# Optimization experiments

Hardware: AMD Instinct MI355X
Metric: run time of the kernel (lower is better)

## Reference

```python
import jax, jax.numpy as jnp
import numpy as np

N_EMBD = 1024
N_HEAD = 16
B, T = 1, 4096
EPS = 1e-5


def layer_norm(x, w):
    mu = jnp.mean(x, axis=-1, keepdims=True)
    var = jnp.var(x, axis=-1, keepdims=True)
    return (x - mu) / jnp.sqrt(var + EPS) * w


def setup_inputs() -> dict:
    key = jax.random.key(0)
    ks = jax.random.split(key, 6)
    s = 0.02
    return {
        "x": jax.random.normal(ks[0], (B, T, N_EMBD), dtype=jnp.float32),
        "w_qkv": jax.random.normal(ks[1], (N_EMBD, 3 * N_EMBD), dtype=jnp.float32) * s,
        "w_attn_proj": jax.random.normal(ks[2], (N_EMBD, N_EMBD), dtype=jnp.float32) * s,
        "w_fc": jax.random.normal(ks[3], (N_EMBD, 4 * N_EMBD), dtype=jnp.float32) * s,
        "w_mlp_proj": jax.random.normal(ks[4], (4 * N_EMBD, N_EMBD), dtype=jnp.float32) * s,
        "ln1_w": jnp.ones((N_EMBD,), dtype=jnp.float32),
        "ln2_w": jnp.ones((N_EMBD,), dtype=jnp.float32),
    }


def reference(x, w_qkv, w_attn_proj, w_fc, w_mlp_proj, ln1_w, ln2_w):
    Bq, Tq, C = x.shape
    hs = C // N_HEAD

    # --- attention branch (pre-norm) ---
    h = layer_norm(x, ln1_w)
    qkv = h @ w_qkv  # [B,T,3C]
    q, k, v = jnp.split(qkv, 3, axis=-1)
    q = q.reshape(Bq, Tq, N_HEAD, hs).transpose(0, 2, 1, 3)  # [B,H,T,hs]
    k = k.reshape(Bq, Tq, N_HEAD, hs).transpose(0, 2, 1, 3)
    v = v.reshape(Bq, Tq, N_HEAD, hs).transpose(0, 2, 1, 3)

    scores = jnp.einsum("bhqd,bhkd->bhqk", q, k) * (1.0 / jnp.sqrt(jnp.float32(hs)))
    causal = jnp.tril(jnp.ones((Tq, Tq), dtype=bool))
    scores = jnp.where(causal, scores, -jnp.inf)
    weights = jax.nn.softmax(scores, axis=-1)  # dropout=0 -> identity
    out = jnp.einsum("bhqk,bhkd->bhqd", weights, v)
    out = out.transpose(0, 2, 1, 3).reshape(Bq, Tq, C)
    x = x + out @ w_attn_proj

    # --- MLP branch (pre-norm) ---
    h = layer_norm(x, ln2_w)
    h = jax.nn.gelu(h @ w_fc, approximate=False)  # nn.GELU default is exact
    x = x + h @ w_mlp_proj
    return x
```

## Files before the change

kernel.cpp:

```cpp
#include <hip/hip_runtime.h>
#include <cstdint>

typedef __attribute__((ext_vector_type(8))) short short8;
typedef __attribute__((ext_vector_type(4))) float f32x4;
typedef __attribute__((ext_vector_type(4))) unsigned int u32x4;

__device__ __forceinline__ float b2f(unsigned short u) {
    return __uint_as_float(((unsigned int)u) << 16);
}
__device__ __forceinline__ unsigned short f2b(float f) {
    unsigned int u = __float_as_uint(f);
    u += 0x7FFFu + ((u >> 16) & 1u);
    return (unsigned short)(u >> 16);
}

__global__ __launch_bounds__(256) void k_transpose_all(
        const float* __restrict__ w0, const float* __restrict__ w1,
        const float* __restrict__ w2, const float* __restrict__ w3,
        unsigned short* __restrict__ o0, unsigned short* __restrict__ o1,
        unsigned short* __restrict__ o2, unsigned short* __restrict__ o3) {
    __shared__ float tile[32][33];
    int b = blockIdx.x;
    const float* w; unsigned short* o; int K, N, nx, tb;
    if (b < 3072)      { w = w0; o = o0; K = 1024; N = 3072; nx = 96;  tb = b; }
    else if (b < 4096) { w = w1; o = o1; K = 1024; N = 1024; nx = 32;  tb = b - 3072; }
    else if (b < 8192) { w = w2; o = o2; K = 1024; N = 4096; nx = 128; tb = b - 4096; }
    else               { w = w3; o = o3; K = 4096; N = 1024; nx = 32;  tb = b - 8192; }
    int n0 = (tb % nx) * 32, k0 = (tb / nx) * 32;
    int tx = threadIdx.x, ty = threadIdx.y;
#pragma unroll
    for (int i = 0; i < 4; i++)
        tile[ty + 8 * i][tx] = w[(size_t)(k0 + ty + 8 * i) * N + n0 + tx];
    __syncthreads();
#pragma unroll
    for (int i = 0; i < 4; i++)
        o[(size_t)(n0 + ty + 8 * i) * K + k0 + tx] = f2b(tile[tx][ty + 8 * i]);
}

__global__ __launch_bounds__(256) void k_layernorm(
        const float* __restrict__ x, const float* __restrict__ w,
        unsigned short* __restrict__ out) {
    int row = blockIdx.x, tid = threadIdx.x;
    const float4* xr = (const float4*)(x + (size_t)row * 1024);
    float4 v = xr[tid];
    float s  = v.x + v.y + v.z + v.w;
    float ss = v.x * v.x + v.y * v.y + v.z * v.z + v.w * v.w;
#pragma unroll
    for (int off = 32; off >= 1; off >>= 1) {
        s  += __shfl_down(s, off);
        ss += __shfl_down(ss, off);
    }
    __shared__ float red[10];
    if ((tid & 63) == 0) { red[tid >> 6] = s; red[4 + (tid >> 6)] = ss; }
    __syncthreads();
    if (tid == 0) {
        float S  = red[0] + red[1] + red[2] + red[3];
        float SS = red[4] + red[5] + red[6] + red[7];
        float mu  = S * (1.0f / 1024.0f);
        float var = SS * (1.0f / 1024.0f) - mu * mu;
        red[8] = mu; red[9] = rsqrtf(var + 1e-5f);
    }
    __syncthreads();
    float mu = red[8], rs = red[9];
    float4 wv = ((const float4*)w)[tid];
    ushort4 pk;
    pk.x = f2b((v.x - mu) * rs * wv.x);
    pk.y = f2b((v.y - mu) * rs * wv.y);
    pk.z = f2b((v.z - mu) * rs * wv.z);
    pk.w = f2b((v.w - mu) * rs * wv.w);
    *(ushort4*)(out + (size_t)row * 1024 + tid * 4) = pk;
}

__global__ __launch_bounds__(256) void k_reduce(
        const float* __restrict__ res, const float* __restrict__ p0,
        const float* __restrict__ p1, float* __restrict__ out, int n4) {
    int i = blockIdx.x * 256 + threadIdx.x;
    if (i < n4) {
        float4 a = ((const float4*)res)[i];
        float4 b = ((const float4*)p0)[i];
        float4 c = ((const float4*)p1)[i];
        a.x += b.x + c.x; a.y += b.y + c.y; a.z += b.z + c.z; a.w += b.w + c.w;
        ((float4*)out)[i] = a;
    }
}

template <int EPI, int TM, int TN, int MINW>
__global__ __launch_bounds__(256, MINW) void k_gemm_bt(
        const unsigned short* __restrict__ A, const unsigned short* __restrict__ BT,
        const float* __restrict__ RES, void* __restrict__ OUT,
        int M, int N, int K) {
    constexpr int WT = (TM == 128) ? 64 : 32;
    constexpr int MI = WT / 16;
    constexpr int NA = TM / 32, NB = TN / 32;
    __shared__ __align__(16) unsigned short As[TM * 64];
    __shared__ __align__(16) unsigned short Bs[TN * 64];
    int tid  = threadIdx.x;
    int lane = tid & 63, wave = tid >> 6;
    int quad = lane >> 4, qr = lane & 15;
    int wm_off = (wave >> 1) * WT;
    int wn_off = (wave & 1) * WT;
    int m0 = blockIdx.y * TM, n0 = blockIdx.x * TN;
    int ks = K / gridDim.z;
    int kbeg = blockIdx.z * ks;
    int r0 = tid >> 3;
    int c0 = (tid & 7) * 8;
    int cs = 8 * (((tid & 7) + (r0 & 7)) & 7);
    int cswz[2];
#pragma unroll
    for (int kk = 0; kk < 2; kk++) cswz[kk] = 8 * (((kk * 4) + quad + (qr & 7)) & 7);

    const unsigned short* Ap = A  + (size_t)(m0 + r0) * K + kbeg + c0;
    const unsigned short* Bp = BT + (size_t)(n0 + r0) * K + kbeg + c0;
    const size_t sA = (size_t)32 * K;

    uint4 pa0, pa1, pa2, pa3, pb0, pb1, pb2, pb3;
    pa0 = *(const uint4*)(Ap);
    pa1 = *(const uint4*)(Ap + sA);
    if constexpr (NA == 4) {
        pa2 = *(const uint4*)(Ap + 2 * sA);
        pa3 = *(const uint4*)(Ap + 3 * sA);
    }
    pb0 = *(const uint4*)(Bp);
    pb1 = *(const uint4*)(Bp + sA);
    if constexpr (NB == 4) {
        pb2 = *(const uint4*)(Bp + 2 * sA);
        pb3 = *(const uint4*)(Bp + 3 * sA);
    }

    f32x4 acc[MI][MI] = {};
    for (int k0 = 0; k0 < ks; k0 += 64) {
        __syncthreads();
        *(uint4*)&As[(r0)      * 64 + cs] = pa0;
        *(uint4*)&As[(32 + r0) * 64 + cs] = pa1;
        if constexpr (NA == 4) {
            *(uint4*)&As[(64 + r0) * 64 + cs] = pa2;
            *(uint4*)&As[(96 + r0) * 64 + cs] = pa3;
        }
        *(uint4*)&Bs[(r0)      * 64 + cs] = pb0;
        *(uint4*)&Bs[(32 + r0) * 64 + cs] = pb1;
        if constexpr (NB == 4) {
            *(uint4*)&Bs[(64 + r0) * 64 + cs] = pb2;
            *(uint4*)&Bs[(96 + r0) * 64 + cs] = pb3;
        }
        __syncthreads();
        if (k0 + 64 < ks) {
            int k = k0 + 64;
            pa0 = *(const uint4*)(Ap + k);
            pa1 = *(const uint4*)(Ap + sA + k);
            if constexpr (NA == 4) {
                pa2 = *(const uint4*)(Ap + 2 * sA + k);
                pa3 = *(const uint4*)(Ap + 3 * sA + k);
            }
            pb0 = *(const uint4*)(Bp + k);
            pb1 = *(const uint4*)(Bp + sA + k);
            if constexpr (NB == 4) {
                pb2 = *(const uint4*)(Bp + 2 * sA + k);
                pb3 = *(const uint4*)(Bp + 3 * sA + k);
            }
        }
#pragma unroll
        for (int kk = 0; kk < 2; kk++) {
            short8 af[MI], bfr[MI];
#pragma unroll
            for (int i = 0; i < MI; i++) af[i]  = *(const short8*)&As[(wm_off + i * 16 + qr) * 64 + cswz[kk]];
#pragma unroll
            for (int j = 0; j < MI; j++) bfr[j] = *(const short8*)&Bs[(wn_off + j * 16 + qr) * 64 + cswz[kk]];
#pragma unroll
            for (int i = 0; i < MI; i++)
#pragma unroll
                for (int j = 0; j < MI; j++)
                    acc[i][j] = __builtin_amdgcn_mfma_f32_16x16x32_bf16(af[i], bfr[j], acc[i][j], 0, 0, 0);
        }
    }
    float* outz = (EPI == 0) ? ((float*)OUT + (size_t)blockIdx.z * M * N) : (float*)OUT;
#pragma unroll
    for (int i = 0; i < MI; i++) {
#pragma unroll
        for (int j = 0; j < MI; j++) {
#pragma unroll
            for (int r = 0; r < 4; r++) {
                int row = m0 + wm_off + i * 16 + quad * 4 + r;
                int col = n0 + wn_off + j * 16 + qr;
                size_t idx = (size_t)row * N + col;
                float v = acc[i][j][r];
                if (EPI == 0)      outz[idx] = v;
                else if (EPI == 1) ((unsigned short*)OUT)[idx] = f2b(v);
                else if (EPI == 2) ((float*)OUT)[idx] = RES[idx] + v;
                else {
                    float u = v * fmaf(v * v, 0.035677408f, 0.79788456f);
                    float e = fminf(u * 2.885390082f, 80.0f);
                    float t = exp2f(e);
                    float g = v * t / (t + 1.0f);
                    ((unsigned short*)OUT)[idx] = f2b(g);
                }
            }
        }
    }
}

__global__ __launch_bounds__(256, 4) void k_attn(
        const unsigned short* __restrict__ qkv, unsigned short* __restrict__ out) {
    __shared__ unsigned short Ks[128][72];
    __shared__ unsigned short Vt[64][136];

    const float C1 = 0.18033688f;
    const float C2 = 5.77078016f;

    int l = blockIdx.x;
    int h = l & 15;
    int qb = 63 - (l >> 4);
    int q0 = qb * 64;

    int tid = threadIdx.x;
    int wave = tid >> 6, lane = tid & 63;
    int lane16 = lane & 15, quad = lane >> 4;
    int qrow = q0 + wave * 16 + lane16;

    {
        int srow = tid >> 2, sc0 = (tid & 3) * 16;
        size_t base = (size_t)(q0 + srow) * 3072 + h * 64 + sc0;
        *(uint4*)&Ks[srow][sc0]     = *(const uint4*)&qkv[base];
        *(uint4*)&Ks[srow][sc0 + 8] = *(const uint4*)&qkv[base + 8];
    }
    __syncthreads();
    short8 aq0 = *(const short8*)&Ks[wave * 16 + lane16][quad * 8];
    short8 aq1 = *(const short8*)&Ks[wave * 16 + lane16][32 + quad * 8];

    f32x4 Oacc[4] = {};
    float lsum = 0.f;

    int srow = tid >> 1, sc0 = (tid & 1) * 32;
    int vk = (lane & 31) * 2;
    int d0 = wave * 16 + (lane >> 5) * 8;
    int u  = lane & 15;
    int tt = ((u & 6) << 1) | ((u & 8) >> 2) | (u & 1);
    int dstc = (lane & 16) * 2 + 2 * tt;

    uint4 pk0, pk1, pk2, pk3, pv0, pv1, pv2, pv3;
    {
        size_t base = (size_t)srow * 3072 + 1024 + h * 64 + sc0;
        pk0 = *(const uint4*)&qkv[base];
        pk1 = *(const uint4*)&qkv[base + 8];
        pk2 = *(const uint4*)&qkv[base + 16];
        pk3 = *(const uint4*)&qkv[base + 24];
        size_t vb0 = (size_t)vk * 3072 + 2048 + h * 64 + d0;
        pv0 = *(const uint4*)&qkv[vb0];
        pv1 = *(const uint4*)&qkv[vb0 + 3072];
        size_t vb1 = (size_t)(64 + vk) * 3072 + 2048 + h * 64 + d0;
        pv2 = *(const uint4*)&qkv[vb1];
        pv3 = *(const uint4*)&qkv[vb1 + 3072];
    }

    for (int kc = 0; kc <= qb; kc += 2) {
        __syncthreads();
        {
            *(uint4*)&Ks[srow][sc0]      = pk0;
            *(uint4*)&Ks[srow][sc0 + 8]  = pk1;
            *(uint4*)&Ks[srow][sc0 + 16] = pk2;
            *(uint4*)&Ks[srow][sc0 + 24] = pk3;
        }
        {
            const unsigned short* pe0 = (const unsigned short*)&pv0;
            const unsigned short* po0 = (const unsigned short*)&pv1;
            const unsigned short* pe1 = (const unsigned short*)&pv2;
            const unsigned short* po1 = (const unsigned short*)&pv3;
#pragma unroll
            for (int j = 0; j < 8; j++) {
                *(uint32_t*)&Vt[d0 + j][dstc]      = (uint32_t)pe0[j] | ((uint32_t)po0[j] << 16);
                *(uint32_t*)&Vt[d0 + j][64 + dstc] = (uint32_t)pe1[j] | ((uint32_t)po1[j] << 16);
            }
        }
        __syncthreads();

        if (kc + 2 <= qb) {
            size_t base = (size_t)((kc + 2) * 64 + srow) * 3072 + 1024 + h * 64 + sc0;
            pk0 = *(const uint4*)&qkv[base];
            pk1 = *(const uint4*)&qkv[base + 8];
            pk2 = *(const uint4*)&qkv[base + 16];
            pk3 = *(const uint4*)&qkv[base + 24];
            size_t vb0 = (size_t)((kc + 2) * 64 + vk) * 3072 + 2048 + h * 64 + d0;
            pv0 = *(const uint4*)&qkv[vb0];
            pv1 = *(const uint4*)&qkv[vb0 + 3072];
            size_t vb1 = (size_t)((kc + 3) * 64 + vk) * 3072 + 2048 + h * 64 + d0;
            pv2 = *(const uint4*)&qkv[vb1];
            pv3 = *(const uint4*)&qkv[vb1 + 3072];
        }

        f32x4 sacc[8] = {};
#pragma unroll
        for (int kt = 0; kt < 8; kt++) {
            short8 bk0 = *(const short8*)&Ks[kt * 16 + lane16][quad * 8];
            short8 bk1 = *(const short8*)&Ks[kt * 16 + lane16][32 + quad * 8];
            sacc[kt] = __builtin_amdgcn_mfma_f32_16x16x32_bf16(bk0, aq0, sacc[kt], 0, 0, 0);
            sacc[kt] = __builtin_amdgcn_mfma_f32_16x16x32_bf16(bk1, aq1, sacc[kt], 0, 0, 0);
        }

        bool domask = (kc + 2 > qb);
        short8 ap[4];
#pragma unroll
        for (int s = 0; s < 4; s++) {
            u32x4 w;
#pragma unroll
            for (int hh = 0; hh < 2; hh++) {
                int kt = 2 * s + hh;
                float pr[4];
#pragma unroll
                for (int r = 0; r < 4; r++) {
                    float sc = sacc[kt][r];
                    if (domask) {
                        int key = kc * 64 + kt * 16 + quad * 4 + r;
                        sc = (key <= qrow) ? sc : -__builtin_inff();
                    }
                    float p = exp2f(fmaf(sc, C1, -C2));
                    lsum += p;
                    pr[r] = p;
                }
                uint32_t w0 = (__float_as_uint(pr[0]) >> 16) | (__float_as_uint(pr[1]) & 0xFFFF0000u);
                uint32_t w1 = (__float_as_uint(pr[2]) >> 16) | (__float_as_uint(pr[3]) & 0xFFFF0000u);
                if (hh == 0) { w.x = w0; w.y = w1; } else { w.z = w0; w.w = w1; }
            }
            ap[s] = __builtin_bit_cast(short8, w);
        }

#pragma unroll
        for (int s = 0; s < 4; s++) {
#pragma unroll
            for (int dt = 0; dt < 4; dt++) {
                short8 bv = *(const short8*)&Vt[dt * 16 + lane16][s * 32 + quad * 8];
                Oacc[dt] = __builtin_amdgcn_mfma_f32_16x16x32_bf16(ap[s], bv, Oacc[dt], 0, 0, 0);
            }
        }
    }

    float lf = lsum;
    lf += __shfl_xor(lf, 16);
    lf += __shfl_xor(lf, 32);
    float invl[4];
#pragma unroll
    for (int r = 0; r < 4; r++) invl[r] = 1.0f / __shfl(lf, quad * 4 + r);
#pragma unroll
    for (int dt = 0; dt < 4; dt++) {
#pragma unroll
        for (int r = 0; r < 4; r++) {
            int qr_out = q0 + wave * 16 + quad * 4 + r;
            out[(size_t)qr_out * 1024 + h * 64 + dt * 16 + lane16] = f2b(Oacc[dt][r] * invl[r]);
        }
    }
}

extern "C" void kernel_launch(void* const* d_in, const int* in_sizes, int n_in,
                              void* d_out, int out_size, void* d_ws, size_t ws_size,
                              hipStream_t stream) {
    const float* x      = (const float*)d_in[0];
    const float* w_qkv  = (const float*)d_in[1];
    const float* w_attn = (const float*)d_in[2];
    const float* w_fc   = (const float*)d_in[3];
    const float* w_mlp  = (const float*)d_in[4];
    const float* ln1w   = (const float*)d_in[5];
    const float* ln2w   = (const float*)d_in[6];

    char* ws = (char*)d_ws;
    unsigned short* h      = (unsigned short*)(ws + 0);
    unsigned short* wqkvT  = (unsigned short*)(ws + 8388608);
    unsigned short* wattnT = (unsigned short*)(ws + 14680064);
    unsigned short* wfcT   = (unsigned short*)(ws + 16777216);
    unsigned short* wmlpT  = (unsigned short*)(ws + 25165824);
    unsigned short* qkv    = (unsigned short*)(ws + 33554432);
    unsigned short* attno  = (unsigned short*)(ws + 58720256);
    float*          x2     = (float*)(ws + 67108864);
    unsigned short* fcact  = (unsigned short*)(ws + 83886080);
    float* pA = (float*)(ws + 83886080);
    float* pM = (float*)(ws + 33554432);
    float* outF = (float*)d_out;

    k_transpose_all<<<12288, dim3(32, 8), 0, stream>>>(
        w_qkv, w_attn, w_fc, w_mlp, wqkvT, wattnT, wfcT, wmlpT);

    k_layernorm<<<4096, 256, 0, stream>>>(x, ln1w, h);
    k_gemm_bt<1, 128, 128, 3><<<dim3(24, 32), 256, 0, stream>>>(h, wqkvT, nullptr, qkv, 4096, 3072, 1024);
    k_attn<<<1024, 256, 0, stream>>>(qkv, attno);
    k_gemm_bt<0, 128, 128, 3><<<dim3(8, 32, 2), 256, 0, stream>>>(attno, wattnT, nullptr, pA, 4096, 1024, 1024);
    k_reduce<<<4096, 256, 0, stream>>>(x, pA, pA + 4194304, x2, 1048576);
    k_layernorm<<<4096, 256, 0, stream>>>(x2, ln2w, h);
    k_gemm_bt<3, 128, 128, 3><<<dim3(32, 32), 256, 0, stream>>>(h, wfcT, nullptr, fcact, 4096, 4096, 1024);
    k_gemm_bt<0, 128, 128, 3><<<dim3(8, 32, 2), 256, 0, stream>>>(fcact, wmlpT, nullptr, pM, 4096, 1024, 4096);
    k_reduce<<<4096, 256, 0, stream>>>(x2, pM, pM + 4194304, outF, 1048576);
}
```

Baseline: 373.6 us.

## Swizzle attention K/V shared-memory layout, rebalance causal block order, add MFMA priority

Replaces the padded K and transposed-V shared-memory arrays with unpadded XOR-swizzled layouts and rewrites the global-load and transpose-store indexing to match, using v_perm to pack V pairs. The aim is to avoid LDS bank conflicts and padding waste. It also reorders the causal query-block schedule into interleaved short and long blocks to balance work across CUs, and raises wave priority around the MFMA loops. The swizzle indexing is intricate and could cause correctness or conflict regressions.

```diff
diff --git a/kernel.cpp b/kernel.cpp
--- a/kernel.cpp
+++ b/kernel.cpp
@@ -200,15 +200,18 @@
 
 __global__ __launch_bounds__(256, 4) void k_attn(
         const unsigned short* __restrict__ qkv, unsigned short* __restrict__ out) {
-    __shared__ unsigned short Ks[128][72];
-    __shared__ unsigned short Vt[64][136];
+    __shared__ __align__(16) unsigned short Ks[128 * 64];
+    __shared__ __align__(16) unsigned short Vt[64 * 128];
 
     const float C1 = 0.18033688f;
     const float C2 = 5.77078016f;
 
     int l = blockIdx.x;
     int h = l & 15;
-    int qb = 63 - (l >> 4);
+    int idx = l >> 4;
+    int kk_ = idx & 15, hi_ = idx >> 4;
+    int qb = (hi_ == 0) ? (2 * kk_) : (hi_ == 1) ? (63 - 2 * kk_)
+           : (hi_ == 2) ? (31 - 2 * kk_) : (32 + 2 * kk_);
     int q0 = qb * 64;
 
     int tid = threadIdx.x;
@@ -217,83 +220,95 @@
     int qrow = q0 + wave * 16 + lane16;
 
     {
-        int srow = tid >> 2, sc0 = (tid & 3) * 16;
-        size_t base = (size_t)(q0 + srow) * 3072 + h * 64 + sc0;
-        *(uint4*)&Ks[srow][sc0]     = *(const uint4*)&qkv[base];
-        *(uint4*)&Ks[srow][sc0 + 8] = *(const uint4*)&qkv[base + 8];
+        int srow = tid >> 2;
+        int c1 = 2 * (tid & 3);
+        int p1 = c1 ^ (srow & 7), p2 = (c1 | 1) ^ (srow & 7);
+        size_t base = (size_t)(q0 + srow) * 3072 + h * 64 + c1 * 8;
+        *(uint4*)&Ks[srow * 64 + p1 * 8] = *(const uint4*)&qkv[base];
+        *(uint4*)&Ks[srow * 64 + p2 * 8] = *(const uint4*)&qkv[base + 8];
     }
     __syncthreads();
-    short8 aq0 = *(const short8*)&Ks[wave * 16 + lane16][quad * 8];
-    short8 aq1 = *(const short8*)&Ks[wave * 16 + lane16][32 + quad * 8];
+    short8 aq0, aq1;
+    {
+        int pq = quad ^ (lane16 & 7);
+        const unsigned short* qr_ = &Ks[(wave * 16 + lane16) * 64];
+        aq0 = *(const short8*)&qr_[pq * 8];
+        aq1 = *(const short8*)&qr_[(pq ^ 4) * 8];
+    }
 
     f32x4 Oacc[4] = {};
     float lsum = 0.f;
 
-    int srow = tid >> 1, sc0 = (tid & 1) * 32;
-    int vk = (lane & 31) * 2;
-    int d0 = wave * 16 + (lane >> 5) * 8;
-    int u  = lane & 15;
-    int tt = ((u & 6) << 1) | ((u & 8) >> 2) | (u & 1);
-    int dstc = (lane & 16) * 2 + 2 * tt;
-
-    uint4 pk0, pk1, pk2, pk3, pv0, pv1, pv2, pv3;
+    int a_ = lane >> 3, b_ = lane & 7;
+    size_t kgbase = (size_t)(wave * 32 + a_) * 3072 + 1024 + h * 64 + ((b_ ^ a_) << 3);
+    int    kwbase = (wave * 32 + a_) * 64 + b_ * 8;
+    size_t vgbase = (size_t)(wave * 32 + 2 * a_) * 3072 + 2048 + h * 64 + (b_ << 3);
+    int tt0 = ((a_ & 6) << 1) | (a_ & 1);
+    int pc0 = wave * 16 + tt0, pc1 = pc0 + 2;
+    int vo0 = ((((pc0 >> 2) ^ b_) & 15) << 4) | ((pc0 & 3) << 2);
+    int vo1 = ((((pc1 >> 2) ^ b_) & 15) << 4) | ((pc1 & 3) << 2);
+
+    uint4 pk0, pk1, pk2, pk3, pvE0, pvO0, pvE1, pvO1;
     {
-        size_t base = (size_t)srow * 3072 + 1024 + h * 64 + sc0;
-        pk0 = *(const uint4*)&qkv[base];
-        pk1 = *(const uint4*)&qkv[base + 8];
-        pk2 = *(const uint4*)&qkv[base + 16];
-        pk3 = *(const uint4*)&qkv[base + 24];
-        size_t vb0 = (size_t)vk * 3072 + 2048 + h * 64 + d0;
-        pv0 = *(const uint4*)&qkv[vb0];
-        pv1 = *(const uint4*)&qkv[vb0 + 3072];
-        size_t vb1 = (size_t)(64 + vk) * 3072 + 2048 + h * 64 + d0;
-        pv2 = *(const uint4*)&qkv[vb1];
-        pv3 = *(const uint4*)&qkv[vb1 + 3072];
+        pk0 = *(const uint4*)&qkv[kgbase];
+        pk1 = *(const uint4*)&qkv[kgbase + 24576];
+        pk2 = *(const uint4*)&qkv[kgbase + 49152];
+        pk3 = *(const uint4*)&qkv[kgbase + 73728];
+        pvE0 = *(const uint4*)&qkv[vgbase];
+        pvO0 = *(const uint4*)&qkv[vgbase + 3072];
+        pvE1 = *(const uint4*)&qkv[vgbase + 49152];
+        pvO1 = *(const uint4*)&qkv[vgbase + 49152 + 3072];
     }
 
     for (int kc = 0; kc <= qb; kc += 2) {
         __syncthreads();
         {
-            *(uint4*)&Ks[srow][sc0]      = pk0;
-            *(uint4*)&Ks[srow][sc0 + 8]  = pk1;
-            *(uint4*)&Ks[srow][sc0 + 16] = pk2;
-            *(uint4*)&Ks[srow][sc0 + 24] = pk3;
+            *(uint4*)&Ks[kwbase]        = pk0;
+            *(uint4*)&Ks[kwbase + 512]  = pk1;
+            *(uint4*)&Ks[kwbase + 1024] = pk2;
+            *(uint4*)&Ks[kwbase + 1536] = pk3;
         }
         {
-            const unsigned short* pe0 = (const unsigned short*)&pv0;
-            const unsigned short* po0 = (const unsigned short*)&pv1;
-            const unsigned short* pe1 = (const unsigned short*)&pv2;
-            const unsigned short* po1 = (const unsigned short*)&pv3;
-#pragma unroll
-            for (int j = 0; j < 8; j++) {
-                *(uint32_t*)&Vt[d0 + j][dstc]      = (uint32_t)pe0[j] | ((uint32_t)po0[j] << 16);
-                *(uint32_t*)&Vt[d0 + j][64 + dstc] = (uint32_t)pe1[j] | ((uint32_t)po1[j] << 16);
+            const uint32_t* e0 = (const uint32_t*)&pvE0;
+            const uint32_t* o0 = (const uint32_t*)&pvO0;
+            const uint32_t* e1 = (const uint32_t*)&pvE1;
+            const uint32_t* o1 = (const uint32_t*)&pvO1;
+            char* vt = (char*)Vt + b_ * 8 * 256;
+#pragma unroll
+            for (int j = 0; j < 4; j++) {
+                *(uint32_t*)(vt + (2 * j) * 256     + vo0) = __builtin_amdgcn_perm(o0[j], e0[j], 0x05040100u);
+                *(uint32_t*)(vt + (2 * j + 1) * 256 + vo0) = __builtin_amdgcn_perm(o0[j], e0[j], 0x07060302u);
+                *(uint32_t*)(vt + (2 * j) * 256     + vo1) = __builtin_amdgcn_perm(o1[j], e1[j], 0x05040100u);
+                *(uint32_t*)(vt + (2 * j + 1) * 256 + vo1) = __builtin_amdgcn_perm(o1[j], e1[j], 0x07060302u);
             }
         }
         __syncthreads();
 
         if (kc + 2 <= qb) {
-            size_t base = (size_t)((kc + 2) * 64 + srow) * 3072 + 1024 + h * 64 + sc0;
-            pk0 = *(const uint4*)&qkv[base];
-            pk1 = *(const uint4*)&qkv[base + 8];
-            pk2 = *(const uint4*)&qkv[base + 16];
-            pk3 = *(const uint4*)&qkv[base + 24];
-            size_t vb0 = (size_t)((kc + 2) * 64 + vk) * 3072 + 2048 + h * 64 + d0;
-            pv0 = *(const uint4*)&qkv[vb0];
-            pv1 = *(const uint4*)&qkv[vb0 + 3072];
-            size_t vb1 = (size_t)((kc + 3) * 64 + vk) * 3072 + 2048 + h * 64 + d0;
-            pv2 = *(const uint4*)&qkv[vb1];
-            pv3 = *(const uint4*)&qkv[vb1 + 3072];
+            size_t kb = kgbase + (size_t)(kc + 2) * 196608;
+            pk0 = *(const uint4*)&qkv[kb];
+            pk1 = *(const uint4*)&qkv[kb + 24576];
+            pk2 = *(const uint4*)&qkv[kb + 49152];
+            pk3 = *(const uint4*)&qkv[kb + 73728];
+            size_t vb = vgbase + (size_t)(kc + 2) * 196608;
+            pvE0 = *(const uint4*)&qkv[vb];
+            pvO0 = *(const uint4*)&qkv[vb + 3072];
+            pvE1 = *(const uint4*)&qkv[vb + 49152];
+            pvO1 = *(const uint4*)&qkv[vb + 49152 + 3072];
         }
 
         f32x4 sacc[8] = {};
+        __builtin_amdgcn_s_setprio(1);
 #pragma unroll
         for (int kt = 0; kt < 8; kt++) {
-            short8 bk0 = *(const short8*)&Ks[kt * 16 + lane16][quad * 8];
-            short8 bk1 = *(const short8*)&Ks[kt * 16 + lane16][32 + quad * 8];
+            int ph = quad ^ (lane16 & 7);
+            const unsigned short* krow = &Ks[(kt * 16 + lane16) * 64];
+            short8 bk0 = *(const short8*)&krow[ph * 8];
+            short8 bk1 = *(const short8*)&krow[(ph ^ 4) * 8];
             sacc[kt] = __builtin_amdgcn_mfma_f32_16x16x32_bf16(bk0, aq0, sacc[kt], 0, 0, 0);
             sacc[kt] = __builtin_amdgcn_mfma_f32_16x16x32_bf16(bk1, aq1, sacc[kt], 0, 0, 0);
         }
+        __builtin_amdgcn_s_setprio(0);
 
         bool domask = (kc + 2 > qb);
         short8 ap[4];
@@ -322,14 +337,18 @@
             ap[s] = __builtin_bit_cast(short8, w);
         }
 
+        __builtin_amdgcn_s_setprio(1);
 #pragma unroll
         for (int s = 0; s < 4; s++) {
 #pragma unroll
             for (int dt = 0; dt < 4; dt++) {
-                short8 bv = *(const short8*)&Vt[dt * 16 + lane16][s * 32 + quad * 8];
+                int dv = dt * 16 + lane16;
+                int blk = (4 * s + quad) ^ (dv >> 3);
+                short8 bv = *(const short8*)((const char*)Vt + dv * 256 + blk * 16);
                 Oacc[dt] = __builtin_amdgcn_mfma_f32_16x16x32_bf16(ap[s], bv, Oacc[dt], 0, 0, 0);
             }
         }
+        __builtin_amdgcn_s_setprio(0);
     }
 
     float lf = lsum;
```

Result: slower. 409.3 us (+9.6%).

## Split attention keys across waves with cross-wave reduction and balanced block order

Applied to the files above, without the earlier changes.

Attention now assigns each wave a 32-key slice of every 128-key chunk for all 64 query rows, instead of 16 query rows against all keys. K is fed to the MFMAs straight from global memory into registers. V is double-buffered in LDS with one barrier per chunk, and the partial outputs and row sums are reduced across waves through LDS at the end. Query blocks are reordered so that long and short causal blocks interleave, and s_setprio hints are added around the MFMA sections. The aim is fewer barriers, no K staging, and better load balance, at the cost of more registers (occupancy hint lowered from 4 to 2) and a serialized final reduction.

```diff
diff --git a/kernel.cpp b/kernel.cpp
--- a/kernel.cpp
+++ b/kernel.cpp
@@ -198,152 +198,215 @@
     }
 }
 
-__global__ __launch_bounds__(256, 4) void k_attn(
+__global__ __launch_bounds__(256, 2) void k_attn(
         const unsigned short* __restrict__ qkv, unsigned short* __restrict__ out) {
-    __shared__ unsigned short Ks[128][72];
-    __shared__ unsigned short Vt[64][136];
+    __shared__ __align__(16) unsigned short Vt[2][64][136];
+    __shared__ float lred[4][64];
 
     const float C1 = 0.18033688f;
     const float C2 = 5.77078016f;
 
     int l = blockIdx.x;
     int h = l & 15;
-    int qb = 63 - (l >> 4);
+    int idx = l >> 4;
+    int kk_ = idx & 15, hi_ = idx >> 4;
+    int qb = (hi_ == 0) ? (2 * kk_) : (hi_ == 1) ? (63 - 2 * kk_)
+           : (hi_ == 2) ? (31 - 2 * kk_) : (32 + 2 * kk_);
     int q0 = qb * 64;
+    int lastc = qb >> 1;
 
     int tid = threadIdx.x;
     int wave = tid >> 6, lane = tid & 63;
     int lane16 = lane & 15, quad = lane >> 4;
-    int qrow = q0 + wave * 16 + lane16;
-
-    {
-        int srow = tid >> 2, sc0 = (tid & 3) * 16;
-        size_t base = (size_t)(q0 + srow) * 3072 + h * 64 + sc0;
-        *(uint4*)&Ks[srow][sc0]     = *(const uint4*)&qkv[base];
-        *(uint4*)&Ks[srow][sc0 + 8] = *(const uint4*)&qkv[base + 8];
-    }
-    __syncthreads();
-    short8 aq0 = *(const short8*)&Ks[wave * 16 + lane16][quad * 8];
-    short8 aq1 = *(const short8*)&Ks[wave * 16 + lane16][32 + quad * 8];
-
-    f32x4 Oacc[4] = {};
-    float lsum = 0.f;
-
-    int srow = tid >> 1, sc0 = (tid & 1) * 32;
+
+    size_t kbase = (size_t)(wave * 32 + lane16) * 3072 + 1024 + h * 64 + quad * 8;
+    size_t qbase = (size_t)(q0 + lane16) * 3072 + h * 64 + quad * 8;
     int vk = (lane & 31) * 2;
     int d0 = wave * 16 + (lane >> 5) * 8;
-    int u  = lane & 15;
+    size_t vgbase = (size_t)vk * 3072 + 2048 + h * 64 + d0;
+    int u = lane & 15;
     int tt = ((u & 6) << 1) | ((u & 8) >> 2) | (u & 1);
     int dstc = (lane & 16) * 2 + 2 * tt;
 
-    uint4 pk0, pk1, pk2, pk3, pv0, pv1, pv2, pv3;
+    uint4 pvE0 = *(const uint4*)&qkv[vgbase];
+    uint4 pvO0 = *(const uint4*)&qkv[vgbase + 3072];
+    uint4 pvE1 = *(const uint4*)&qkv[vgbase + 196608];
+    uint4 pvO1 = *(const uint4*)&qkv[vgbase + 196608 + 3072];
+    uint4 kp00 = *(const uint4*)&qkv[kbase];
+    uint4 kp01 = *(const uint4*)&qkv[kbase + 32];
+    uint4 kp10 = *(const uint4*)&qkv[kbase + 49152];
+    uint4 kp11 = *(const uint4*)&qkv[kbase + 49152 + 32];
+    short8 aq[4][2];
+#pragma unroll
+    for (int g = 0; g < 4; g++) {
+        aq[g][0] = __builtin_bit_cast(short8, *(const uint4*)&qkv[qbase + g * 49152]);
+        aq[g][1] = __builtin_bit_cast(short8, *(const uint4*)&qkv[qbase + g * 49152 + 32]);
+    }
     {
-        size_t base = (size_t)srow * 3072 + 1024 + h * 64 + sc0;
-        pk0 = *(const uint4*)&qkv[base];
-        pk1 = *(const uint4*)&qkv[base + 8];
-        pk2 = *(const uint4*)&qkv[base + 16];
-        pk3 = *(const uint4*)&qkv[base + 24];
-        size_t vb0 = (size_t)vk * 3072 + 2048 + h * 64 + d0;
-        pv0 = *(const uint4*)&qkv[vb0];
-        pv1 = *(const uint4*)&qkv[vb0 + 3072];
-        size_t vb1 = (size_t)(64 + vk) * 3072 + 2048 + h * 64 + d0;
-        pv2 = *(const uint4*)&qkv[vb1];
-        pv3 = *(const uint4*)&qkv[vb1 + 3072];
-    }
-
-    for (int kc = 0; kc <= qb; kc += 2) {
+        const unsigned short* pe0 = (const unsigned short*)&pvE0;
+        const unsigned short* po0 = (const unsigned short*)&pvO0;
+        const unsigned short* pe1 = (const unsigned short*)&pvE1;
+        const unsigned short* po1 = (const unsigned short*)&pvO1;
+#pragma unroll
+        for (int j = 0; j < 8; j++) {
+            *(uint32_t*)&Vt[0][d0 + j][dstc]      = (uint32_t)pe0[j] | ((uint32_t)po0[j] << 16);
+            *(uint32_t*)&Vt[0][d0 + j][64 + dstc] = (uint32_t)pe1[j] | ((uint32_t)po1[j] << 16);
+        }
+    }
+    if (lastc >= 1) {
+        size_t vb = vgbase + 393216;
+        pvE0 = *(const uint4*)&qkv[vb];
+        pvO0 = *(const uint4*)&qkv[vb + 3072];
+        pvE1 = *(const uint4*)&qkv[vb + 196608];
+        pvO1 = *(const uint4*)&qkv[vb + 196608 + 3072];
+    }
+
+    f32x4 Oacc[4][4] = {};
+    float lsum[4] = {0.f, 0.f, 0.f, 0.f};
+
+    for (int c = 0; c <= lastc; ++c) {
+        int cur = c & 1;
         __syncthreads();
-        {
-            *(uint4*)&Ks[srow][sc0]      = pk0;
-            *(uint4*)&Ks[srow][sc0 + 8]  = pk1;
-            *(uint4*)&Ks[srow][sc0 + 16] = pk2;
-            *(uint4*)&Ks[srow][sc0 + 24] = pk3;
-        }
-        {
-            const unsigned short* pe0 = (const unsigned short*)&pv0;
-            const unsigned short* po0 = (const unsigned short*)&pv1;
-            const unsigned short* pe1 = (const unsigned short*)&pv2;
-            const unsigned short* po1 = (const unsigned short*)&pv3;
+
+        f32x4 sacc[2][4];
+        __builtin_amdgcn_s_setprio(1);
+#pragma unroll
+        for (int kg = 0; kg < 2; kg++) {
+            short8 a0 = __builtin_bit_cast(short8, kg ? kp10 : kp00);
+            short8 a1 = __builtin_bit_cast(short8, kg ? kp11 : kp01);
+#pragma unroll
+            for (int g = 0; g < 4; g++) {
+                f32x4 s = {};
+                s = __builtin_amdgcn_mfma_f32_16x16x32_bf16(a0, aq[g][0], s, 0, 0, 0);
+                s = __builtin_amdgcn_mfma_f32_16x16x32_bf16(a1, aq[g][1], s, 0, 0, 0);
+                sacc[kg][g] = s;
+            }
+        }
+        __builtin_amdgcn_s_setprio(0);
+
+        if (c < lastc) {
+            const unsigned short* pe0 = (const unsigned short*)&pvE0;
+            const unsigned short* po0 = (const unsigned short*)&pvO0;
+            const unsigned short* pe1 = (const unsigned short*)&pvE1;
+            const unsigned short* po1 = (const unsigned short*)&pvO1;
 #pragma unroll
             for (int j = 0; j < 8; j++) {
-                *(uint32_t*)&Vt[d0 + j][dstc]      = (uint32_t)pe0[j] | ((uint32_t)po0[j] << 16);
-                *(uint32_t*)&Vt[d0 + j][64 + dstc] = (uint32_t)pe1[j] | ((uint32_t)po1[j] << 16);
-            }
-        }
-        __syncthreads();
-
-        if (kc + 2 <= qb) {
-            size_t base = (size_t)((kc + 2) * 64 + srow) * 3072 + 1024 + h * 64 + sc0;
-            pk0 = *(const uint4*)&qkv[base];
-            pk1 = *(const uint4*)&qkv[base + 8];
-            pk2 = *(const uint4*)&qkv[base + 16];
-            pk3 = *(const uint4*)&qkv[base + 24];
-            size_t vb0 = (size_t)((kc + 2) * 64 + vk) * 3072 + 2048 + h * 64 + d0;
-            pv0 = *(const uint4*)&qkv[vb0];
-            pv1 = *(const uint4*)&qkv[vb0 + 3072];
-            size_t vb1 = (size_t)((kc + 3) * 64 + vk) * 3072 + 2048 + h * 64 + d0;
-            pv2 = *(const uint4*)&qkv[vb1];
-            pv3 = *(const uint4*)&qkv[vb1 + 3072];
-        }
-
-        f32x4 sacc[8] = {};
-#pragma unroll
-        for (int kt = 0; kt < 8; kt++) {
-            short8 bk0 = *(const short8*)&Ks[kt * 16 + lane16][quad * 8];
-            short8 bk1 = *(const short8*)&Ks[kt * 16 + lane16][32 + quad * 8];
-            sacc[kt] = __builtin_amdgcn_mfma_f32_16x16x32_bf16(bk0, aq0, sacc[kt], 0, 0, 0);
-            sacc[kt] = __builtin_amdgcn_mfma_f32_16x16x32_bf16(bk1, aq1, sacc[kt], 0, 0, 0);
-        }
-
-        bool domask = (kc + 2 > qb);
+                *(uint32_t*)&Vt[cur ^ 1][d0 + j][dstc]      = (uint32_t)pe0[j] | ((uint32_t)po0[j] << 16);
+                *(uint32_t*)&Vt[cur ^ 1][d0 + j][64 + dstc] = (uint32_t)pe1[j] | ((uint32_t)po1[j] << 16);
+            }
+        }
+        if (c < lastc) {
+            size_t kb = kbase + (size_t)(c + 1) * 393216;
+            kp00 = *(const uint4*)&qkv[kb];
+            kp01 = *(const uint4*)&qkv[kb + 32];
+            kp10 = *(const uint4*)&qkv[kb + 49152];
+            kp11 = *(const uint4*)&qkv[kb + 49152 + 32];
+        }
+        if (c + 2 <= lastc) {
+            size_t vb = vgbase + (size_t)(c + 2) * 393216;
+            pvE0 = *(const uint4*)&qkv[vb];
+            pvO0 = *(const uint4*)&qkv[vb + 3072];
+            pvE1 = *(const uint4*)&qkv[vb + 196608];
+            pvO1 = *(const uint4*)&qkv[vb + 196608 + 3072];
+        }
+
+        int keybase = c * 128 + wave * 32;
+        bool domask = (keybase + 31 > q0);
         short8 ap[4];
 #pragma unroll
-        for (int s = 0; s < 4; s++) {
+        for (int g = 0; g < 4; g++) {
+            int qrow = q0 + g * 16 + lane16;
             u32x4 w;
 #pragma unroll
-            for (int hh = 0; hh < 2; hh++) {
-                int kt = 2 * s + hh;
+            for (int kg = 0; kg < 2; kg++) {
                 float pr[4];
 #pragma unroll
                 for (int r = 0; r < 4; r++) {
-                    float sc = sacc[kt][r];
+                    float sc = sacc[kg][g][r];
                     if (domask) {
-                        int key = kc * 64 + kt * 16 + quad * 4 + r;
+                        int key = keybase + kg * 16 + quad * 4 + r;
                         sc = (key <= qrow) ? sc : -__builtin_inff();
                     }
                     float p = exp2f(fmaf(sc, C1, -C2));
-                    lsum += p;
+                    lsum[g] += p;
                     pr[r] = p;
                 }
                 uint32_t w0 = (__float_as_uint(pr[0]) >> 16) | (__float_as_uint(pr[1]) & 0xFFFF0000u);
                 uint32_t w1 = (__float_as_uint(pr[2]) >> 16) | (__float_as_uint(pr[3]) & 0xFFFF0000u);
-                if (hh == 0) { w.x = w0; w.y = w1; } else { w.z = w0; w.w = w1; }
-            }
-            ap[s] = __builtin_bit_cast(short8, w);
-        }
-
-#pragma unroll
-        for (int s = 0; s < 4; s++) {
-#pragma unroll
-            for (int dt = 0; dt < 4; dt++) {
-                short8 bv = *(const short8*)&Vt[dt * 16 + lane16][s * 32 + quad * 8];
-                Oacc[dt] = __builtin_amdgcn_mfma_f32_16x16x32_bf16(ap[s], bv, Oacc[dt], 0, 0, 0);
-            }
-        }
-    }
-
-    float lf = lsum;
-    lf += __shfl_xor(lf, 16);
-    lf += __shfl_xor(lf, 32);
-    float invl[4];
-#pragma unroll
-    for (int r = 0; r < 4; r++) invl[r] = 1.0f / __shfl(lf, quad * 4 + r);
-#pragma unroll
-    for (int dt = 0; dt < 4; dt++) {
-#pragma unroll
-        for (int r = 0; r < 4; r++) {
-            int qr_out = q0 + wave * 16 + quad * 4 + r;
-            out[(size_t)qr_out * 1024 + h * 64 + dt * 16 + lane16] = f2b(Oacc[dt][r] * invl[r]);
+                if (kg == 0) { w.x = w0; w.y = w1; } else { w.z = w0; w.w = w1; }
+            }
+            ap[g] = __builtin_bit_cast(short8, w);
+        }
+
+        __builtin_amdgcn_s_setprio(1);
+#pragma unroll
+        for (int dt = 0; dt < 4; dt++) {
+            short8 bv = *(const short8*)&Vt[cur][dt * 16 + lane16][wave * 32 + quad * 8];
+#pragma unroll
+            for (int g = 0; g < 4; g++)
+                Oacc[g][dt] = __builtin_amdgcn_mfma_f32_16x16x32_bf16(ap[g], bv, Oacc[g][dt], 0, 0, 0);
+        }
+        __builtin_amdgcn_s_setprio(0);
+    }
+
+#pragma unroll
+    for (int g = 0; g < 4; g++) {
+        float lf = lsum[g];
+        lf += __shfl_xor(lf, 16);
+        lf += __shfl_xor(lf, 32);
+        lsum[g] = lf;
+    }
+    if (quad == 0) {
+#pragma unroll
+        for (int g = 0; g < 4; g++) lred[wave][g * 16 + lane16] = lsum[g];
+    }
+    __syncthreads();
+
+    float* Obuf = (float*)&Vt[0][0][0];
+    if (wave == 3) {
+#pragma unroll
+        for (int g = 0; g < 4; g++)
+#pragma unroll
+            for (int dt = 0; dt < 4; dt++)
+#pragma unroll
+                for (int r = 0; r < 4; r++)
+                    Obuf[(g * 16 + quad * 4 + r) * 68 + dt * 16 + lane16] = Oacc[g][dt][r];
+    }
+    __syncthreads();
+    if (wave == 2) {
+#pragma unroll
+        for (int g = 0; g < 4; g++)
+#pragma unroll
+            for (int dt = 0; dt < 4; dt++)
+#pragma unroll
+                for (int r = 0; r < 4; r++)
+                    Obuf[(g * 16 + quad * 4 + r) * 68 + dt * 16 + lane16] += Oacc[g][dt][r];
+    }
+    __syncthreads();
+    if (wave == 1) {
+#pragma unroll
+        for (int g = 0; g < 4; g++)
+#pragma unroll
+            for (int dt = 0; dt < 4; dt++)
+#pragma unroll
+                for (int r = 0; r < 4; r++)
+                    Obuf[(g * 16 + quad * 4 + r) * 68 + dt * 16 + lane16] += Oacc[g][dt][r];
+    }
+    __syncthreads();
+    if (wave == 0) {
+#pragma unroll
+        for (int g = 0; g < 4; g++) {
+#pragma unroll
+            for (int r = 0; r < 4; r++) {
+                int q = g * 16 + quad * 4 + r;
+                float lt = lred[0][q] + lred[1][q] + lred[2][q] + lred[3][q];
+                float inv = 1.0f / lt;
+#pragma unroll
+                for (int dt = 0; dt < 4; dt++) {
+                    float v = Oacc[g][dt][r] + Obuf[q * 68 + dt * 16 + lane16];
+                    out[(size_t)(q0 + q) * 1024 + h * 64 + dt * 16 + lane16] = f2b(v * inv);
+                }
+            }
         }
     }
 }
```

New measurement: 405.9 us. 8.6% more time.
